# Optimization experiments

Measured on AMD Instinct MI355X. Metric: run time of the kernel, lower is better.

## Reference

```python
import jax, jax.numpy as jnp
import numpy as np

B, S, D_MODEL, H = 2, 2048, 1024, 16
HD = D_MODEL // H  # 64
EPS = 1e-6


def setup_inputs() -> dict:
    key = jax.random.key(0)
    ks = jax.random.split(key, 8)
    x = jax.random.normal(ks[0], (B, S, D_MODEL), dtype=jnp.float32)
    # Proper RoPE rotation angles: theta_i = pos / 10000^(2i/head_dim)
    inv_freq = 1.0 / (10000.0 ** (np.arange(0, HD, 2, dtype=np.float32) / HD))  # (HD/2,)
    angles = np.arange(S, dtype=np.float32)[:, None] * inv_freq[None, :]        # (S, HD/2)
    rope_cos = jnp.asarray(np.cos(angles))
    rope_sin = jnp.asarray(np.sin(angles))
    w_std = 1.0 / np.sqrt(D_MODEL)
    wq = jax.random.normal(ks[1], (D_MODEL, D_MODEL), dtype=jnp.float32) * w_std
    wk = jax.random.normal(ks[2], (D_MODEL, D_MODEL), dtype=jnp.float32) * w_std
    wv = jax.random.normal(ks[3], (D_MODEL, D_MODEL), dtype=jnp.float32) * w_std
    wo = jax.random.normal(ks[4], (D_MODEL, D_MODEL), dtype=jnp.float32) * w_std
    q_scale = 1.0 + 0.02 * jax.random.normal(ks[5], (HD,), dtype=jnp.float32)
    k_scale = 1.0 + 0.02 * jax.random.normal(ks[6], (HD,), dtype=jnp.float32)
    return {"x": x, "wq": wq, "wk": wk, "wv": wv, "wo": wo,
            "q_scale": q_scale, "k_scale": k_scale,
            "rope_cos": rope_cos, "rope_sin": rope_sin}


def _rmsnorm(t, scale):
    # RMSNorm over head_dim
    var = jnp.mean(jnp.square(t), axis=-1, keepdims=True)
    return t * jax.lax.rsqrt(var + EPS) * scale


def _apply_rope(t, cos, sin):
    # t: (B,S,H,HD); interpret consecutive pairs as complex (real, imag)
    b, s, h, d = t.shape
    tp = t.reshape(b, s, h, d // 2, 2)
    tr, ti = tp[..., 0], tp[..., 1]
    c = cos[None, :, None, :]  # (1,S,1,HD/2)
    sn = sin[None, :, None, :]
    or_ = tr * c - ti * sn
    oi = tr * sn + ti * c
    return jnp.stack([or_, oi], axis=-1).reshape(b, s, h, d)


def reference(x, wq, wk, wv, wo, q_scale, k_scale, rope_cos, rope_sin):
    b, s, _ = x.shape
    # Torch-style linear: y = x @ W^T, W is (out, in)
    q = jnp.einsum('bsd,od->bso', x, wq).reshape(b, s, H, HD)
    k = jnp.einsum('bsd,od->bso', x, wk).reshape(b, s, H, HD)
    v = jnp.einsum('bsd,od->bso', x, wv).reshape(b, s, H, HD)
    q = _apply_rope(_rmsnorm(q, q_scale), rope_cos, rope_sin)
    k = _apply_rope(_rmsnorm(k, k_scale), rope_cos, rope_sin)
    # scaled dot-product attention (no mask), fp32 softmax
    scale = 1.0 / np.sqrt(HD)
    scores = jnp.einsum('bqhd,bkhd->bhqk', q, k) * scale
    probs = jax.nn.softmax(scores.astype(jnp.float32), axis=-1)
    attn = jnp.einsum('bhqk,bkhd->bqhd', probs, v).reshape(b, s, D_MODEL)
    return jnp.einsum('bso,do->bsd', attn, wo.T).astype(x.dtype) if False else jnp.einsum('bsd,od->bso', attn, wo)
```

## Files before the change

kernel.cpp:

```cpp
#include <hip/hip_runtime.h>
#include <hip/hip_bf16.h>


#define B_ 2
#define S_ 2048
#define D_ 1024
#define H_ 16
#define HD_ 64
#define M_ (B_*S_)

typedef __attribute__((ext_vector_type(8))) short short8;
typedef __attribute__((ext_vector_type(4))) short short4v;
typedef __attribute__((ext_vector_type(4))) float f32x4;
typedef __attribute__((ext_vector_type(4))) _Float16 half4;

static __device__ __forceinline__ short f2bf(float f) {
    __hip_bfloat16 h = __float2bfloat16(f);
    return *reinterpret_cast<short*>(&h);
}
static __device__ __forceinline__ short f2h(float f) {
    _Float16 h = (_Float16)f;
    return *reinterpret_cast<short*>(&h);
}
static __device__ __forceinline__ float bf2f(short s) {
    unsigned u = ((unsigned)(unsigned short)s) << 16;
    float f; __builtin_memcpy(&f, &u, 4); return f;
}

typedef __attribute__((address_space(1))) const unsigned int gu32_t;
typedef __attribute__((address_space(3))) unsigned int lu32_t;
static __device__ __forceinline__ void gld16(const short* g, short* l) {
    __builtin_amdgcn_global_load_lds((gu32_t*)g, (lu32_t*)l, 16, 0, 0);
}

__global__ __launch_bounds__(256)
void convert_bf16(const float* __restrict__ x,
                  const float* __restrict__ wq, const float* __restrict__ wk,
                  const float* __restrict__ wv, const float* __restrict__ wo,
                  short* __restrict__ xb, short* __restrict__ wqkvb, short* __restrict__ wob)
{
    const size_t t4 = ((size_t)blockIdx.x * 256 + threadIdx.x) * 4;
    const float* src; short* dst; size_t off, doff;
    if (t4 < 4194304)      { src = x;  dst = xb;    off = t4;           doff = t4; }
    else if (t4 < 5242880) { src = wq; dst = wqkvb; off = t4 - 4194304; doff = t4 - 4194304; }
    else if (t4 < 6291456) { src = wk; dst = wqkvb; off = t4 - 5242880; doff = t4 - 4194304; }
    else if (t4 < 7340032) { src = wv; dst = wqkvb; off = t4 - 6291456; doff = t4 - 4194304; }
    else                   { src = wo; dst = wob;   off = t4 - 7340032; doff = t4 - 7340032; }
    float4 v = *(const float4*)(src + off);
    short4v s = { f2bf(v.x), f2bf(v.y), f2bf(v.z), f2bf(v.w) };
    *(short4v*)(dst + doff) = s;
}

template<int EPI>
__global__ __launch_bounds__(256)
void gemm_bf16(const short* __restrict__ A, const short* __restrict__ Bw,
               short* __restrict__ Qb, short* __restrict__ Kb,
               short* __restrict__ Vt, float* __restrict__ Cout)
{
    __shared__ __align__(16) short As[128*32];
    __shared__ __align__(16) short Bs[128*32];
    const int tid = threadIdx.x;
    const int w = tid >> 6, lane = tid & 63, quad = lane >> 4, l16 = lane & 15;
    const int wr = w >> 1, wc = w & 1;
    const int bm0 = blockIdx.x * 128, bn0 = blockIdx.y * 128;

    const int srow = tid >> 2;
    const int skch = (tid & 3) * 8;
    const short* gA0 = A  + (size_t)(bm0 + srow) * 1024 + skch;
    const short* gA1 = A  + (size_t)(bm0 + 64 + srow) * 1024 + skch;
    const short* gB0 = Bw + (size_t)(bn0 + srow) * 1024 + skch;
    const short* gB1 = Bw + (size_t)(bn0 + 64 + srow) * 1024 + skch;
    short* lA0 = As + w*512;
    short* lA1 = As + 2048 + w*512;
    short* lB0 = Bs + w*512;
    short* lB1 = Bs + 2048 + w*512;

    f32x4 acc[4][4];
    #pragma unroll
    for (int i = 0; i < 4; ++i)
        #pragma unroll
        for (int j = 0; j < 4; ++j) acc[i][j] = (f32x4){0.f,0.f,0.f,0.f};

    for (int k0 = 0; k0 < 1024; k0 += 32) {
        __syncthreads();
        gld16(gA0 + k0, lA0);
        gld16(gA1 + k0, lA1);
        gld16(gB0 + k0, lB0);
        gld16(gB1 + k0, lB1);
        __syncthreads();
        short8 af[4], bfr[4];
        #pragma unroll
        for (int i = 0; i < 4; ++i)
            af[i] = *(const short8*)(As + (wr*64 + i*16 + l16)*32 + quad*8);
        #pragma unroll
        for (int j = 0; j < 4; ++j)
            bfr[j] = *(const short8*)(Bs + (wc*64 + j*16 + l16)*32 + quad*8);
        #pragma unroll
        for (int i = 0; i < 4; ++i)
            #pragma unroll
            for (int j = 0; j < 4; ++j)
                acc[i][j] = __builtin_amdgcn_mfma_f32_16x16x32_bf16(af[i], bfr[j], acc[i][j], 0, 0, 0);
    }

    #pragma unroll
    for (int i = 0; i < 4; ++i) {
        #pragma unroll
        for (int r = 0; r < 4; ++r) {
            const int m = bm0 + wr*64 + i*16 + quad*4 + r;
            #pragma unroll
            for (int j = 0; j < 4; ++j) {
                const int n = bn0 + wc*64 + j*16 + l16;
                const float v = acc[i][j][r];
                if (EPI == 0) {
                    const int which = n >> 10, nn = n & 1023;
                    const int h = nn >> 6, hd = nn & 63;
                    const int b = m >> 11, s = m & (S_-1);
                    if (which == 0)      Qb[(((size_t)b*H_ + h)*S_ + s)*HD_ + hd] = f2bf(v);
                    else if (which == 1) Kb[(((size_t)b*H_ + h)*S_ + s)*HD_ + hd] = f2bf(v);
                    else                 Vt[(((size_t)b*H_ + h)*HD_ + hd)*S_ + s] = f2h(v);
                } else {
                    Cout[(size_t)m*1024 + n] = v;
                }
            }
        }
    }
}

__global__ __launch_bounds__(256)
void rmsnorm_rope(short* __restrict__ qbh, short* __restrict__ kbh,
                  const float* __restrict__ q_scale, const float* __restrict__ k_scale,
                  const float* __restrict__ rope_cos, const float* __restrict__ rope_sin)
{
    const int lane = threadIdx.x & 63;
    const int wid  = threadIdx.x >> 6;
    const int row  = blockIdx.x * 4 + wid;
    const bool isq = (blockIdx.y == 0);
    short* t = isq ? qbh : kbh;
    const float* sc = isq ? q_scale : k_scale;
    const int s = row & (S_-1);
    float v = bf2f(t[(size_t)row * HD_ + lane]);
    float ssum = v * v;
    #pragma unroll
    for (int m = 32; m >= 1; m >>= 1) ssum += __shfl_xor(ssum, m, 64);
    float r = rsqrtf(ssum * (1.0f/64.0f) + 1e-6f);
    float nv = v * r * sc[lane];
    const int p = lane >> 1;
    float c  = rope_cos[s*32 + p];
    float sn = rope_sin[s*32 + p];
    float partner = __shfl_xor(nv, 1, 64);
    float outv = (lane & 1) ? (partner * sn + nv * c) : (nv * c - partner * sn);
    if (isq) outv *= 0.18033688011112042f;
    t[(size_t)row * HD_ + lane] = f2bf(outv);
}

__global__ __launch_bounds__(256, 2)
void flash_mfma(const short* __restrict__ qb, const short* __restrict__ kb,
                const short* __restrict__ vt, short* __restrict__ attnb)
{
    __shared__ __align__(16) short Ks[64*64];
    __shared__ __align__(16) short Vs[64*64];

    const int tid  = threadIdx.x;
    const int wv   = tid >> 6;
    const int lane = tid & 63;
    const int quad = lane >> 4;
    const int l16  = lane & 15;
    const int bh   = blockIdx.y;
    const int b    = bh >> 4, h = bh & (H_-1);
    const int q0   = blockIdx.x * 128 + wv * 32;
    const size_t hbase = (size_t)bh * S_ * HD_;
    const size_t vbase = (size_t)bh * HD_ * S_;

    short8 qfrag[2][2];
    #pragma unroll
    for (int qf = 0; qf < 2; ++qf)
        #pragma unroll
        for (int c = 0; c < 2; ++c)
            qfrag[qf][c] = *(const short8*)(qb + hbase + (size_t)(q0 + qf*16 + l16)*HD_ + c*32 + quad*8);

    f32x4 Oacc[2][4];
    #pragma unroll
    for (int qf = 0; qf < 2; ++qf)
        #pragma unroll
        for (int dt = 0; dt < 4; ++dt) Oacc[qf][dt] = (f32x4){0.f,0.f,0.f,0.f};
    float l_lane[2] = {0.f, 0.f};

    #pragma unroll 1
    for (int kt = 0; kt < S_; kt += 64) {
        __syncthreads();
        #pragma unroll
        for (int c = tid; c < 512; c += 256) {
            const int key = c >> 3, dch = c & 7;
            *(short8*)(Ks + key*64 + ((dch ^ (key & 7)) << 3)) =
                *(const short8*)(kb + hbase + (size_t)(kt + key)*HD_ + dch*8);
        }
        #pragma unroll
        for (int c = tid; c < 512; c += 256) {
            const int d = c >> 3, kch = c & 7;
            *(short8*)(Vs + d*64 + ((kch ^ (d & 7)) << 3)) =
                *(const short8*)(vt + vbase + (size_t)d*S_ + kt + kch*8);
        }
        __syncthreads();

        #pragma unroll
        for (int st = 0; st < 4; ++st) {
            short8 kf0 = *(const short8*)(Ks + (st*16 + l16)*64 + (((quad    ) ^ (l16 & 7)) << 3));
            short8 kf1 = *(const short8*)(Ks + (st*16 + l16)*64 + (((4 + quad) ^ (l16 & 7)) << 3));
            #pragma unroll
            for (int qf = 0; qf < 2; ++qf) {
                f32x4 acc = (f32x4){0.f,0.f,0.f,0.f};
                acc = __builtin_amdgcn_mfma_f32_16x16x32_bf16(kf0, qfrag[qf][0], acc, 0, 0, 0);
                acc = __builtin_amdgcn_mfma_f32_16x16x32_bf16(kf1, qfrag[qf][1], acc, 0, 0, 0);
                half4 pb;
                #pragma unroll
                for (int r = 0; r < 4; ++r) {
                    float p = __builtin_amdgcn_exp2f(acc[r] - 12.0f);
                    l_lane[qf] += p;
                    pb[r] = (_Float16)p;
                }
                const int ch16 = st*2 + (quad >> 1);
                const int sw   = ((ch16 ^ (l16 & 7)) << 3) + (quad & 1)*4;
                #pragma unroll
                for (int dt = 0; dt < 4; ++dt) {
                    half4 va = *(const half4*)(Vs + (dt*16 + l16)*64 + sw);
                    Oacc[qf][dt] = __builtin_amdgcn_mfma_f32_16x16x16f16(va, pb, Oacc[qf][dt], 0, 0, 0);
                }
            }
        }
    }

    #pragma unroll
    for (int qf = 0; qf < 2; ++qf) {
        l_lane[qf] += __shfl_xor(l_lane[qf], 16, 64);
        l_lane[qf] += __shfl_xor(l_lane[qf], 32, 64);
        l_lane[qf] = 1.0f / l_lane[qf];
    }
    #pragma unroll
    for (int qf = 0; qf < 2; ++qf) {
        const int s = q0 + qf*16 + l16;
        #pragma unroll
        for (int dt = 0; dt < 4; ++dt) {
            short4v o;
            #pragma unroll
            for (int r = 0; r < 4; ++r) o[r] = f2bf(Oacc[qf][dt][r] * l_lane[qf]);
            *(short4v*)(attnb + (((size_t)b*S_ + s)*H_ + h)*HD_ + dt*16 + quad*4) = o;
        }
    }
}

extern "C" void kernel_launch(void* const* d_in, const int* in_sizes, int n_in,
                              void* d_out, int out_size, void* d_ws, size_t ws_size,
                              hipStream_t stream)
{
    (void)in_sizes; (void)n_in; (void)out_size; (void)ws_size;
    const float* x        = (const float*)d_in[0];
    const float* wq       = (const float*)d_in[1];
    const float* wk       = (const float*)d_in[2];
    const float* wv       = (const float*)d_in[3];
    const float* wo       = (const float*)d_in[4];
    const float* q_scale  = (const float*)d_in[5];
    const float* k_scale  = (const float*)d_in[6];
    const float* rope_cos = (const float*)d_in[7];
    const float* rope_sin = (const float*)d_in[8];
    float* out = (float*)d_out;
    short* ws  = (short*)d_ws;

    short* qbh   = ws;
    short* kbh   = ws + 4194304;
    short* vt    = ws + 8388608;
    short* attnb = ws + 12582912;
    short* xb    = ws + 16777216;
    short* wqkvb = ws + 20971520;
    short* wob   = ws + 24117248;

    convert_bf16<<<dim3(8192), 256, 0, stream>>>(x, wq, wk, wv, wo, xb, wqkvb, wob);
    gemm_bf16<0><<<dim3(M_/128, 24), 256, 0, stream>>>(xb, wqkvb, qbh, kbh, vt, nullptr);
    rmsnorm_rope<<<dim3(B_*H_*S_/4, 2), 256, 0, stream>>>(qbh, kbh, q_scale, k_scale, rope_cos, rope_sin);
    flash_mfma<<<dim3(S_/128, B_*H_), 256, 0, stream>>>(qbh, kbh, vt, attnb);
    gemm_bf16<1><<<dim3(M_/128, 8), 256, 0, stream>>>(attnb, wob, nullptr, nullptr, nullptr, out);
}
```

Measured before the change: 235.6 us.

## Split attention over key halves, register-prefetch K/V, shrink output GEMM tiles

The flash attention kernel now splits the key range into two halves across a third grid dimension. Each half writes unnormalized fp16 partial outputs and row sums, and a new combine kernel adds them and normalizes. The K/V tile loads are prefetched into registers one iteration ahead so global latency overlaps compute. The output projection uses a separate GEMM with 64-row tiles to double the block count. Together these aim to raise occupancy on the many-CU GPU, but they add an extra kernel launch plus partial-result traffic, and the fp16 partial storage may cost accuracy.

```diff
diff --git a/kernel.cpp b/kernel.cpp
--- a/kernel.cpp
+++ b/kernel.cpp
@@ -21,6 +21,9 @@
 static __device__ __forceinline__ short f2h(float f) {
     _Float16 h = (_Float16)f;
     return *reinterpret_cast<short*>(&h);
+}
+static __device__ __forceinline__ float h2f(short s) {
+    _Float16 h; __builtin_memcpy(&h, &s, 2); return (float)h;
 }
 static __device__ __forceinline__ float bf2f(short s) {
     unsigned u = ((unsigned)(unsigned short)s) << 16;
@@ -51,11 +54,9 @@
     *(short4v*)(dst + doff) = s;
 }
 
-template<int EPI>
-__global__ __launch_bounds__(256)
-void gemm_bf16(const short* __restrict__ A, const short* __restrict__ Bw,
-               short* __restrict__ Qb, short* __restrict__ Kb,
-               short* __restrict__ Vt, float* __restrict__ Cout)
+__global__ __launch_bounds__(256)
+void gemm_qkv(const short* __restrict__ A, const short* __restrict__ Bw,
+              short* __restrict__ Qb, short* __restrict__ Kb, short* __restrict__ Vt)
 {
     __shared__ __align__(16) short As[128*32];
     __shared__ __align__(16) short Bs[128*32];
@@ -111,19 +112,74 @@
             for (int j = 0; j < 4; ++j) {
                 const int n = bn0 + wc*64 + j*16 + l16;
                 const float v = acc[i][j][r];
-                if (EPI == 0) {
-                    const int which = n >> 10, nn = n & 1023;
-                    const int h = nn >> 6, hd = nn & 63;
-                    const int b = m >> 11, s = m & (S_-1);
-                    if (which == 0)      Qb[(((size_t)b*H_ + h)*S_ + s)*HD_ + hd] = f2bf(v);
-                    else if (which == 1) Kb[(((size_t)b*H_ + h)*S_ + s)*HD_ + hd] = f2bf(v);
-                    else                 Vt[(((size_t)b*H_ + h)*HD_ + hd)*S_ + s] = f2h(v);
-                } else {
-                    Cout[(size_t)m*1024 + n] = v;
-                }
+                const int which = n >> 10, nn = n & 1023;
+                const int h = nn >> 6, hd = nn & 63;
+                const int b = m >> 11, s = m & (S_-1);
+                if (which == 0)      Qb[(((size_t)b*H_ + h)*S_ + s)*HD_ + hd] = f2bf(v);
+                else if (which == 1) Kb[(((size_t)b*H_ + h)*S_ + s)*HD_ + hd] = f2bf(v);
+                else                 Vt[(((size_t)b*H_ + h)*HD_ + hd)*S_ + s] = f2h(v);
             }
         }
     }
+}
+
+__global__ __launch_bounds__(256)
+void gemm_out(const short* __restrict__ A, const short* __restrict__ Bw,
+              float* __restrict__ C)
+{
+    __shared__ __align__(16) short As[64*32];
+    __shared__ __align__(16) short Bs[128*32];
+    const int tid = threadIdx.x;
+    const int w = tid >> 6, lane = tid & 63, quad = lane >> 4, l16 = lane & 15;
+    const int bm0 = blockIdx.x * 64, bn0 = blockIdx.y * 128;
+
+    const int srow = tid >> 2;
+    const int skch = (tid & 3) * 8;
+    const short* gA  = A  + (size_t)(bm0 + srow) * 1024 + skch;
+    const short* gB0 = Bw + (size_t)(bn0 + srow) * 1024 + skch;
+    const short* gB1 = Bw + (size_t)(bn0 + 64 + srow) * 1024 + skch;
+    short* lA  = As + w*512;
+    short* lB0 = Bs + w*512;
+    short* lB1 = Bs + 2048 + w*512;
+
+    f32x4 acc[4][2];
+    #pragma unroll
+    for (int i = 0; i < 4; ++i) {
+        acc[i][0] = (f32x4){0.f,0.f,0.f,0.f};
+        acc[i][1] = (f32x4){0.f,0.f,0.f,0.f};
+    }
+
+    for (int k0 = 0; k0 < 1024; k0 += 32) {
+        __syncthreads();
+        gld16(gA  + k0, lA);
+        gld16(gB0 + k0, lB0);
+        gld16(gB1 + k0, lB1);
+        __syncthreads();
+        short8 af[4], bfr[2];
+        #pragma unroll
+        for (int i = 0; i < 4; ++i)
+            af[i] = *(const short8*)(As + (i*16 + l16)*32 + quad*8);
+        #pragma unroll
+        for (int j = 0; j < 2; ++j)
+            bfr[j] = *(const short8*)(Bs + (w*32 + j*16 + l16)*32 + quad*8);
+        #pragma unroll
+        for (int i = 0; i < 4; ++i)
+            #pragma unroll
+            for (int j = 0; j < 2; ++j)
+                acc[i][j] = __builtin_amdgcn_mfma_f32_16x16x32_bf16(af[i], bfr[j], acc[i][j], 0, 0, 0);
+    }
+
+    #pragma unroll
+    for (int i = 0; i < 4; ++i)
+        #pragma unroll
+        for (int r = 0; r < 4; ++r) {
+            const int m = bm0 + i*16 + quad*4 + r;
+            #pragma unroll
+            for (int j = 0; j < 2; ++j) {
+                const int n = bn0 + w*32 + j*16 + l16;
+                C[(size_t)m*1024 + n] = acc[i][j][r];
+            }
+        }
 }
 
 __global__ __launch_bounds__(256)
@@ -155,7 +211,7 @@
 
 __global__ __launch_bounds__(256, 2)
 void flash_mfma(const short* __restrict__ qb, const short* __restrict__ kb,
-                const short* __restrict__ vt, short* __restrict__ attnb)
+                const short* __restrict__ vt, short* __restrict__ po, float* __restrict__ pl)
 {
     __shared__ __align__(16) short Ks[64*64];
     __shared__ __align__(16) short Vs[64*64];
@@ -168,8 +224,15 @@
     const int bh   = blockIdx.y;
     const int b    = bh >> 4, h = bh & (H_-1);
     const int q0   = blockIdx.x * 128 + wv * 32;
+    const int sp   = blockIdx.z;
+    const int kt0  = sp * 1024;
     const size_t hbase = (size_t)bh * S_ * HD_;
     const size_t vbase = (size_t)bh * HD_ * S_;
+    short* po_sp = po + (size_t)sp * 4194304;
+    float* pl_sp = pl + (size_t)sp * 65536;
+
+    const int c0r = tid >> 3,       c0c = tid & 7;
+    const int c1r = (tid+256) >> 3, c1c = (tid+256) & 7;
 
     short8 qfrag[2][2];
     #pragma unroll
@@ -185,22 +248,26 @@
         for (int dt = 0; dt < 4; ++dt) Oacc[qf][dt] = (f32x4){0.f,0.f,0.f,0.f};
     float l_lane[2] = {0.f, 0.f};
 
+    short8 rk0 = *(const short8*)(kb + hbase + (size_t)(kt0 + c0r)*HD_ + c0c*8);
+    short8 rk1 = *(const short8*)(kb + hbase + (size_t)(kt0 + c1r)*HD_ + c1c*8);
+    short8 rv0 = *(const short8*)(vt + vbase + (size_t)c0r*S_ + kt0 + c0c*8);
+    short8 rv1 = *(const short8*)(vt + vbase + (size_t)c1r*S_ + kt0 + c1c*8);
+
     #pragma unroll 1
-    for (int kt = 0; kt < S_; kt += 64) {
-        __syncthreads();
-        #pragma unroll
-        for (int c = tid; c < 512; c += 256) {
-            const int key = c >> 3, dch = c & 7;
-            *(short8*)(Ks + key*64 + ((dch ^ (key & 7)) << 3)) =
-                *(const short8*)(kb + hbase + (size_t)(kt + key)*HD_ + dch*8);
-        }
-        #pragma unroll
-        for (int c = tid; c < 512; c += 256) {
-            const int d = c >> 3, kch = c & 7;
-            *(short8*)(Vs + d*64 + ((kch ^ (d & 7)) << 3)) =
-                *(const short8*)(vt + vbase + (size_t)d*S_ + kt + kch*8);
-        }
-        __syncthreads();
+    for (int t = 0; t < 16; ++t) {
+        __syncthreads();
+        *(short8*)(Ks + c0r*64 + ((c0c ^ (c0r & 7)) << 3)) = rk0;
+        *(short8*)(Ks + c1r*64 + ((c1c ^ (c1r & 7)) << 3)) = rk1;
+        *(short8*)(Vs + c0r*64 + ((c0c ^ (c0r & 7)) << 3)) = rv0;
+        *(short8*)(Vs + c1r*64 + ((c1c ^ (c1r & 7)) << 3)) = rv1;
+        __syncthreads();
+        if (t < 15) {
+            const int ktn = kt0 + (t+1)*64;
+            rk0 = *(const short8*)(kb + hbase + (size_t)(ktn + c0r)*HD_ + c0c*8);
+            rk1 = *(const short8*)(kb + hbase + (size_t)(ktn + c1r)*HD_ + c1c*8);
+            rv0 = *(const short8*)(vt + vbase + (size_t)c0r*S_ + ktn + c0c*8);
+            rv1 = *(const short8*)(vt + vbase + (size_t)c1r*S_ + ktn + c1c*8);
+        }
 
         #pragma unroll
         for (int st = 0; st < 4; ++st) {
@@ -233,7 +300,7 @@
     for (int qf = 0; qf < 2; ++qf) {
         l_lane[qf] += __shfl_xor(l_lane[qf], 16, 64);
         l_lane[qf] += __shfl_xor(l_lane[qf], 32, 64);
-        l_lane[qf] = 1.0f / l_lane[qf];
+        if (quad == 0) pl_sp[(size_t)bh*S_ + q0 + qf*16 + l16] = l_lane[qf];
     }
     #pragma unroll
     for (int qf = 0; qf < 2; ++qf) {
@@ -242,10 +309,31 @@
         for (int dt = 0; dt < 4; ++dt) {
             short4v o;
             #pragma unroll
-            for (int r = 0; r < 4; ++r) o[r] = f2bf(Oacc[qf][dt][r] * l_lane[qf]);
-            *(short4v*)(attnb + (((size_t)b*S_ + s)*H_ + h)*HD_ + dt*16 + quad*4) = o;
-        }
-    }
+            for (int r = 0; r < 4; ++r) o[r] = f2h(Oacc[qf][dt][r]);
+            *(short4v*)(po_sp + (((size_t)b*S_ + s)*H_ + h)*HD_ + dt*16 + quad*4) = o;
+        }
+    }
+}
+
+__global__ __launch_bounds__(256)
+void flash_combine(const short* __restrict__ po, const float* __restrict__ pl,
+                   short* __restrict__ attnb)
+{
+    const size_t idx4 = ((size_t)blockIdx.x * 256 + threadIdx.x) * 4;
+    const size_t row  = idx4 >> 6;
+    const int h  = (int)(row & 15);
+    const size_t bs = row >> 4;
+    const int b  = (int)(bs >> 11);
+    const int s  = (int)(bs & (S_-1));
+    const int bh = b*16 + h;
+    const float l = pl[(size_t)bh*S_ + s] + pl[65536 + (size_t)bh*S_ + s];
+    const float inv = 1.0f / l;
+    short4v a0 = *(const short4v*)(po + idx4);
+    short4v a1 = *(const short4v*)(po + 4194304 + idx4);
+    short4v o;
+    #pragma unroll
+    for (int i = 0; i < 4; ++i) o[i] = f2bf((h2f(a0[i]) + h2f(a1[i])) * inv);
+    *(short4v*)(attnb + idx4) = o;
 }
 
 extern "C" void kernel_launch(void* const* d_in, const int* in_sizes, int n_in,
@@ -272,10 +360,13 @@
     short* xb    = ws + 16777216;
     short* wqkvb = ws + 20971520;
     short* wob   = ws + 24117248;
+    short* po    = ws + 25165824;
+    float* pl    = (float*)(ws + 33554432);
 
     convert_bf16<<<dim3(8192), 256, 0, stream>>>(x, wq, wk, wv, wo, xb, wqkvb, wob);
-    gemm_bf16<0><<<dim3(M_/128, 24), 256, 0, stream>>>(xb, wqkvb, qbh, kbh, vt, nullptr);
+    gemm_qkv<<<dim3(M_/128, 24), 256, 0, stream>>>(xb, wqkvb, qbh, kbh, vt);
     rmsnorm_rope<<<dim3(B_*H_*S_/4, 2), 256, 0, stream>>>(qbh, kbh, q_scale, k_scale, rope_cos, rope_sin);
-    flash_mfma<<<dim3(S_/128, B_*H_), 256, 0, stream>>>(qbh, kbh, vt, attnb);
-    gemm_bf16<1><<<dim3(M_/128, 8), 256, 0, stream>>>(attnb, wob, nullptr, nullptr, nullptr, out);
-}
+    flash_mfma<<<dim3(S_/128, B_*H_, 2), 256, 0, stream>>>(qbh, kbh, vt, po, pl);
+    flash_combine<<<dim3(4096), 256, 0, stream>>>(po, pl, attnb);
+    gemm_out<<<dim3(M_/64, D_/128), 256, 0, stream>>>(attnb, wob, out);
+}
```

Result: faster. 225.7 us (-4.2%).
